# Kernel tuning notes

Measured on AMD Instinct MI355X. Metric: run time of the kernel, lower is better.

The kernel has to match this reference:

```python
import jax, jax.numpy as jnp
import numpy as np
from jax import lax

DIM, D_INNER, D_STATE, D_CONV, DT_RANK = 256, 512, 16, 4, 16
B_, H_, W_ = 4, 64, 64


def setup_inputs() -> dict:
    key = jax.random.key(0)
    ks = jax.random.split(key, 10)
    s = lambda k, shape, scale: (jax.random.normal(k, shape, dtype=jnp.float32) * scale)
    inp = {
        "x": s(ks[0], (B_, DIM, H_, W_), 1.0),
        "in_proj_w": s(ks[1], (2 * D_INNER, DIM), DIM ** -0.5),
        "conv_w": s(ks[2], (D_INNER, 1, D_CONV), D_CONV ** -0.5),
        "conv_b": s(ks[3], (D_INNER,), 0.02),
        "x_proj_w": s(ks[4], (DT_RANK + 2 * D_STATE, D_INNER), D_INNER ** -0.5),
        "dt_proj_w": s(ks[5], (D_INNER, DT_RANK), DT_RANK ** -0.5),
        "dt_proj_b": s(ks[6], (D_INNER,), 0.02),
        # A_log init: log(arange(1..d_state)) broadcast over channels (standard S4D-real init)
        "A_log": jnp.broadcast_to(jnp.log(jnp.arange(1, D_STATE + 1, dtype=jnp.float32)), (D_INNER, D_STATE)).copy(),
        "D": jnp.ones((D_INNER,), dtype=jnp.float32),
        "out_proj_w": s(ks[7], (DIM, D_INNER), D_INNER ** -0.5),
    }
    return inp


def _mamba_forward(x, in_proj_w, conv_w, conv_b, x_proj_w, dt_proj_w, dt_proj_b, A_log, D, out_proj_w):
    b, c, h, w = x.shape
    L = h * w
    xs = x.reshape(b, c, L).transpose(0, 2, 1)                      # [b, L, dim]

    xz = jnp.einsum('bld,ed->ble', xs, in_proj_w)                   # [b, L, 2*d_inner]
    u, res = jnp.split(xz, 2, axis=-1)                              # each [b, L, d_inner]

    # causal depthwise conv1d over sequence
    u_t = u.transpose(0, 2, 1)                                      # [b, d_inner, L]
    u_t = lax.conv_general_dilated(u_t, conv_w, window_strides=(1,),
                                   padding=[(D_CONV - 1, 0)],
                                   feature_group_count=D_INNER,
                                   dimension_numbers=('NCH', 'OIH', 'NCH'))
    u = jax.nn.silu(u_t.transpose(0, 2, 1) + conv_b)                # [b, L, d_inner]

    dbc = jnp.einsum('bld,ed->ble', u, x_proj_w)                    # [b, L, dt_rank+2n]
    dt, Bm, Cm = jnp.split(dbc, [DT_RANK, DT_RANK + D_STATE], axis=-1)
    delta = jax.nn.softplus(jnp.einsum('blr,dr->bld', dt, dt_proj_w) + dt_proj_b)  # [b,L,d_inner]

    A = -jnp.exp(A_log)                                             # [d_inner, n]
    deltaA = jnp.exp(jnp.einsum('bld,dn->bldn', delta, A))          # [b,L,d,n]
    deltaBu = jnp.einsum('bld,bln,bld->bldn', delta, Bm, u)         # [b,L,d,n]

    def step(state, inp):
        dA, dBu, c_t = inp                                          # [b,d,n],[b,d,n],[b,n]
        state = dA * state + dBu
        y = jnp.einsum('bdn,bn->bd', state, c_t)
        return state, y

    init = jnp.zeros((b, D_INNER, D_STATE), dtype=x.dtype)
    _, ys = lax.scan(step, init, (jnp.moveaxis(deltaA, 1, 0),
                                  jnp.moveaxis(deltaBu, 1, 0),
                                  jnp.moveaxis(Cm, 1, 0)))
    y = jnp.moveaxis(ys, 0, 1) + u * D                              # [b, L, d_inner]
    y = y * jax.nn.silu(res)
    out = jnp.einsum('ble,de->bld', y, out_proj_w)                  # [b, L, dim]
    return out.transpose(0, 2, 1).reshape(b, c, h, w)


def reference(x, in_proj_w, conv_w, conv_b, x_proj_w, dt_proj_w, dt_proj_b, A_log, D, out_proj_w):
    return _mamba_forward(x, in_proj_w, conv_w, conv_b, x_proj_w, dt_proj_w, dt_proj_b, A_log, D, out_proj_w)
```

## Files before the change

kernel.cpp:

```cpp
#include <hip/hip_runtime.h>
#include <math.h>


namespace {
constexpr int kB   = 4;
constexpr int kDim = 256;
constexpr int kL   = 4096;
constexpr int kDI  = 512;
constexpr int kN   = 16;
constexpr int kNC  = 64;
constexpr int kCS  = 64;
}

typedef __attribute__((ext_vector_type(8))) short bf16x8;
typedef __attribute__((ext_vector_type(4))) float f32x4;
typedef __attribute__((ext_vector_type(2))) float f32x2;

__device__ __forceinline__ float rcpf(float x) { return __builtin_amdgcn_rcpf(x); }
__device__ __forceinline__ float siluf(float x) { return x * rcpf(1.f + __expf(-x)); }
__device__ __forceinline__ float softplusf(float x) {
  return fmaxf(x, 0.f) + __logf(1.f + __expf(-fabsf(x)));
}

__device__ __forceinline__ unsigned short f2bf(float x) {
  union { float f; unsigned int u; } v; v.f = x;
  unsigned int u = v.u;
  u += 0x7fffu + ((u >> 16) & 1u);
  return (unsigned short)(u >> 16);
}
__device__ __forceinline__ float bf2f(unsigned short u) {
  union { unsigned int i; float f; } v; v.i = ((unsigned int)u) << 16; return v.f;
}

__device__ __forceinline__ void gload_lds16(const void* g, void* l) {
  __builtin_amdgcn_global_load_lds(
      (const __attribute__((address_space(1))) unsigned int*)g,
      (__attribute__((address_space(3))) unsigned int*)l, 16, 0, 0);
}

__global__ __launch_bounds__(256) void k_prep(const float* __restrict__ w_in,
                                              const float* __restrict__ w_out,
                                              const float* __restrict__ w_x,
                                              const float* __restrict__ w_dt,
                                              const float* __restrict__ A_log,
                                              const float* __restrict__ x,
                                              unsigned short* __restrict__ wib,
                                              unsigned short* __restrict__ wob,
                                              unsigned short* __restrict__ wxb,
                                              unsigned short* __restrict__ wdtb,
                                              float* __restrict__ Avz,
                                              unsigned int* __restrict__ flagA,
                                              unsigned short* __restrict__ xt) {
  __shared__ float Xs[64][65];
  const int blk = blockIdx.x;
  const int t = threadIdx.x;
  if (blk < 1760) {
    int idx = blk * 256 + t;
    if (idx < 262144) wib[idx] = f2bf(w_in[idx]);
    else if (idx < 393216) wob[idx - 262144] = f2bf(w_out[idx - 262144]);
    else if (idx < 417792) wxb[idx - 393216] = f2bf(w_x[idx - 393216]);
    else {
      int i = idx - 417792;
      int r = i & 31, d = i >> 5;
      wdtb[i] = (r < 16) ? f2bf(w_dt[d * 16 + r]) : (unsigned short)0;
    }
  } else if (blk < 1762) {
    int d = (blk - 1760) * 256 + t;
    float a0 = -__expf(A_log[d * kN]);
    bool ok = true;
#pragma unroll
    for (int n = 1; n < kN; ++n) {
      float av = -__expf(A_log[d * kN + n]);
      ok = ok && (fabsf(av - (n + 1) * a0) <= 1e-5f * fabsf(av));
    }
    Avz[d] = a0;
    unsigned long long bal = __ballot(ok);
    int wv = t >> 6;
    if ((t & 63) == 0) ((unsigned long long*)Xs)[wv] = bal;
    __syncthreads();
    if (t == 0) {
      unsigned long long all = ~0ull;
#pragma unroll
      for (int w = 0; w < 4; ++w) all &= ((unsigned long long*)Xs)[w];
      flagA[blk - 1760] = (all == ~0ull) ? 1u : 0u;
    }
  } else {
    int id = blk - 1762;
    int lb = id & 63, db = (id >> 6) & 3, b = id >> 8;
    const int d0 = db * 64, l0 = lb * 64;
    {
      int lq = (t & 15) * 4;
      int dr = t >> 4;
#pragma unroll
      for (int rep = 0; rep < 4; ++rep) {
        int dd = rep * 16 + dr;
        float4 v = *(const float4*)&x[((size_t)b * kDim + d0 + dd) * kL + l0 + lq];
        Xs[dd][lq] = v.x; Xs[dd][lq + 1] = v.y;
        Xs[dd][lq + 2] = v.z; Xs[dd][lq + 3] = v.w;
      }
    }
    __syncthreads();
    {
      int di = (t & 15) * 4;
      int lr = t >> 4;
#pragma unroll
      for (int rep = 0; rep < 4; ++rep) {
        int lj = rep * 16 + lr;
        ushort4 o;
        o.x = f2bf(Xs[di][lj]);     o.y = f2bf(Xs[di + 1][lj]);
        o.z = f2bf(Xs[di + 2][lj]); o.w = f2bf(Xs[di + 3][lj]);
        *(ushort4*)(xt + ((size_t)b * kL + l0 + lj) * kDim + d0 + di) = o;
      }
    }
  }
}

__global__ __launch_bounds__(256) void gemm_in_lm(const unsigned short* __restrict__ xt,
                                                  const unsigned short* __restrict__ W,
                                                  unsigned short* __restrict__ ubf,
                                                  unsigned short* __restrict__ resb) {
  __shared__ __align__(16) unsigned short As[128 * 64];
  __shared__ __align__(16) unsigned short Bs[128 * 64];
  const int e0 = blockIdx.x * 128;
  const int l0 = blockIdx.y * 128;
  const int b  = blockIdx.z;
  const int t  = threadIdx.x;
  const int wave = t >> 6, lane = t & 63;
  const int wm = wave >> 1, wn = wave & 1;
  const unsigned short* Ab = xt + (size_t)b * kL * kDim;

  f32x4 acc[4][4];
#pragma unroll
  for (int i = 0; i < 4; ++i)
#pragma unroll
    for (int j = 0; j < 4; ++j) acc[i][j] = (f32x4)0.0f;

  const int srow = t >> 3, sch = t & 7;
  for (int kt = 0; kt < 4; ++kt) {
    const int k0 = kt * 64;
#pragma unroll
    for (int c = 0; c < 4; ++c) {
      int row = c * 32 + srow;
      int gch = sch ^ (row & 7);
      gload_lds16(Ab + (size_t)(l0 + row) * kDim + k0 + gch * 8,
                  (char*)As + c * 4096 + wave * 1024);
      gload_lds16(W  + (size_t)(e0 + row) * kDim + k0 + gch * 8,
                  (char*)Bs + c * 4096 + wave * 1024);
    }
    __syncthreads();
#pragma unroll
    for (int ks = 0; ks < 2; ++ks) {
      bf16x8 af[4], bfr[4];
#pragma unroll
      for (int f = 0; f < 4; ++f) {
        int ra = wm * 64 + f * 16 + (lane & 15);
        int ca = (ks * 4 + (lane >> 4)) ^ (ra & 7);
        af[f] = *(const bf16x8*)((const char*)As + ra * 128 + ca * 16);
        int rb = wn * 64 + f * 16 + (lane & 15);
        int cb = (ks * 4 + (lane >> 4)) ^ (rb & 7);
        bfr[f] = *(const bf16x8*)((const char*)Bs + rb * 128 + cb * 16);
      }
#pragma unroll
      for (int i = 0; i < 4; ++i)
#pragma unroll
        for (int j = 0; j < 4; ++j)
          acc[i][j] = __builtin_amdgcn_mfma_f32_16x16x32_bf16(af[i], bfr[j], acc[i][j], 0, 0, 0);
    }
    __syncthreads();
  }

  const bool is_u = (e0 < kDI);
  unsigned short* dst = is_u ? ubf : resb;
  const int ebase = is_u ? e0 : (e0 - kDI);
#pragma unroll
  for (int i = 0; i < 4; ++i)
#pragma unroll
    for (int j = 0; j < 4; ++j)
#pragma unroll
      for (int r = 0; r < 4; ++r) {
        int l = l0 + wm * 64 + i * 16 + (lane >> 4) * 4 + r;
        int e = ebase + wn * 64 + j * 16 + (lane & 15);
        dst[((size_t)b * kL + l) * kDI + e] = f2bf(acc[i][j][r]);
      }
}

__global__ __launch_bounds__(256) void k_xproj_dt(const unsigned short* __restrict__ Wx,
                                                  const unsigned short* __restrict__ Wdtb,
                                                  const float* __restrict__ bdt,
                                                  const unsigned short* __restrict__ ubf,
                                                  const float* __restrict__ cw,
                                                  const float* __restrict__ cb,
                                                  float* __restrict__ dbcBC,
                                                  unsigned short* __restrict__ ucb,
                                                  unsigned short* __restrict__ delb) {
  __shared__ __align__(16) unsigned short As[64 * 64];
  __shared__ __align__(16) unsigned short Bs[64 * 64];
  __shared__ __align__(16) unsigned short dtTl[64 * 32];
  __shared__ __align__(16) unsigned short Wl[128 * 32];
  const int l0 = blockIdx.x * 64;
  const int b  = blockIdx.y;
  const int t  = threadIdx.x;
  const int wave = t >> 6, lane = t & 63;
  const unsigned short* Ub = ubf + (size_t)b * kL * kDI;

  f32x4 acc[3];
#pragma unroll
  for (int i = 0; i < 3; ++i) acc[i] = (f32x4)0.0f;

  const int srow = t >> 3, sch = t & 7;
  for (int kt = 0; kt < 8; ++kt) {
    const int k0 = kt * 64;
#pragma unroll
    for (int c = 0; c < 2; ++c) {
      int row = c * 32 + srow;
      int grow = row < 48 ? row : 47;
      int gch = sch ^ (row & 7);
      gload_lds16(Wx + (size_t)grow * kDI + k0 + gch * 8,
                  (char*)As + c * 4096 + wave * 1024);
    }
#pragma unroll
    for (int c = 0; c < 2; ++c) {
      int row = c * 32 + srow;
      int gch = sch ^ (row & 7);
      int gl = l0 + row;
      int d0 = k0 + gch * 8;
      const unsigned short* base = Ub + (size_t)gl * kDI + d0;
      uint4 zero4 = make_uint4(0, 0, 0, 0);
      uint4 c0v = *(const uint4*)base;
      uint4 c1v = (gl >= 1) ? *(const uint4*)(base - kDI)     : zero4;
      uint4 c2v = (gl >= 2) ? *(const uint4*)(base - 2 * kDI) : zero4;
      uint4 c3v = (gl >= 3) ? *(const uint4*)(base - 3 * kDI) : zero4;
      const unsigned int* p0 = (const unsigned int*)&c0v;
      const unsigned int* p1 = (const unsigned int*)&c1v;
      const unsigned int* p2 = (const unsigned int*)&c2v;
      const unsigned int* p3 = (const unsigned int*)&c3v;
      unsigned short ov[8];
#pragma unroll
      for (int cc = 0; cc < 8; ++cc) {
        int q = cc >> 1, hi = cc & 1;
        float u0 = bf2f((unsigned short)(hi ? (p0[q] >> 16) : (p0[q] & 0xffff)));
        float u1 = bf2f((unsigned short)(hi ? (p1[q] >> 16) : (p1[q] & 0xffff)));
        float u2 = bf2f((unsigned short)(hi ? (p2[q] >> 16) : (p2[q] & 0xffff)));
        float u3 = bf2f((unsigned short)(hi ? (p3[q] >> 16) : (p3[q] & 0xffff)));
        float4 w = *(const float4*)(cw + (d0 + cc) * 4);
        float a = cb[d0 + cc] + w.x * u3 + w.y * u2 + w.z * u1 + w.w * u0;
        ov[cc] = f2bf(siluf(a));
      }
      *(uint4*)((char*)Bs + c * 4096 + t * 16) = *(const uint4*)ov;
      *(uint4*)(ucb + ((size_t)b * kL + gl) * kDI + d0) = *(const uint4*)ov;
    }
    __syncthreads();
#pragma unroll
    for (int ks = 0; ks < 2; ++ks) {
      bf16x8 af[3], bfr;
#pragma unroll
      for (int f = 0; f < 3; ++f) {
        int ra = f * 16 + (lane & 15);
        int ca = (ks * 4 + (lane >> 4)) ^ (ra & 7);
        af[f] = *(const bf16x8*)((const char*)As + ra * 128 + ca * 16);
      }
      int rb = wave * 16 + (lane & 15);
      int cbk = (ks * 4 + (lane >> 4)) ^ (rb & 7);
      bfr = *(const bf16x8*)((const char*)Bs + rb * 128 + cbk * 16);
#pragma unroll
      for (int i = 0; i < 3; ++i)
        acc[i] = __builtin_amdgcn_mfma_f32_16x16x32_bf16(af[i], bfr, acc[i], 0, 0, 0);
    }
    __syncthreads();
  }

#pragma unroll
  for (int i = 1; i < 3; ++i)
#pragma unroll
    for (int r = 0; r < 4; ++r) {
      int m = i * 16 + (lane >> 4) * 4 + r;
      int l = l0 + wave * 16 + (lane & 15);
      dbcBC[((size_t)b * 32 + (m - 16)) * kL + l] = acc[i][r];
    }
  {
    int lloc = wave * 16 + (lane & 15);
    int m0 = (lane >> 4) * 4;
    ushort4 v;
    v.x = f2bf(acc[0][0]); v.y = f2bf(acc[0][1]);
    v.z = f2bf(acc[0][2]); v.w = f2bf(acc[0][3]);
    int byte = lloc * 64 + (((m0 >> 3) ^ (lloc & 3)) << 4) + ((m0 & 7) << 1);
    *(ushort4*)((char*)dtTl + byte) = v;
  }
  if (t < 128) {
    int lz = t >> 1, zc = 2 + (t & 1);
    *(uint4*)((char*)dtTl + lz * 64 + ((zc ^ (lz & 3)) << 4)) = make_uint4(0, 0, 0, 0);
  }
  __syncthreads();

  for (int dt4 = 0; dt4 < 4; ++dt4) {
#pragma unroll
    for (int c2 = 0; c2 < 2; ++c2) {
      int unit = c2 * 256 + t;
      int row = unit >> 2, sc = unit & 3;
      int gch = sc ^ (row & 3);
      gload_lds16(Wdtb + (size_t)(dt4 * 128 + row) * 32 + gch * 8,
                  (char*)Wl + c2 * 4096 + t * 16);
    }
    __syncthreads();
    f32x4 acc2[4][2];
#pragma unroll
    for (int i = 0; i < 4; ++i)
#pragma unroll
      for (int j = 0; j < 2; ++j) acc2[i][j] = (f32x4)0.0f;
    bf16x8 afr[4], bfr2[2];
#pragma unroll
    for (int f = 0; f < 4; ++f) {
      int ra = f * 16 + (lane & 15);
      afr[f] = *(const bf16x8*)((const char*)dtTl + ra * 64 + (((lane >> 4) ^ (ra & 3)) << 4));
    }
#pragma unroll
    for (int f = 0; f < 2; ++f) {
      int rb = wave * 32 + f * 16 + (lane & 15);
      bfr2[f] = *(const bf16x8*)((const char*)Wl + rb * 64 + (((lane >> 4) ^ (rb & 3)) << 4));
    }
#pragma unroll
    for (int i = 0; i < 4; ++i)
#pragma unroll
      for (int j = 0; j < 2; ++j)
        acc2[i][j] = __builtin_amdgcn_mfma_f32_16x16x32_bf16(afr[i], bfr2[j], acc2[i][j], 0, 0, 0);
#pragma unroll
    for (int j = 0; j < 2; ++j) {
      int d = dt4 * 128 + wave * 32 + j * 16 + (lane & 15);
      float bd = bdt[d];
#pragma unroll
      for (int i = 0; i < 4; ++i)
#pragma unroll
        for (int r = 0; r < 4; ++r) {
          int l = l0 + i * 16 + (lane >> 4) * 4 + r;
          float delta = softplusf(acc2[i][j][r] + bd);
          delb[((size_t)b * kL + l) * kDI + d] = f2bf(delta);
        }
    }
    __syncthreads();
  }
}

__global__ __launch_bounds__(128) void k_scanA(const unsigned short* __restrict__ delb,
                                               const unsigned short* __restrict__ ucb,
                                               const float* __restrict__ dbcBC,
                                               const float* __restrict__ A_log,
                                               const float* __restrict__ Avz,
                                               const unsigned int* __restrict__ flagA,
                                               float* __restrict__ Pprod,
                                               float* __restrict__ Pfull,
                                               float* __restrict__ S) {
  __shared__ __align__(16) float Bsh[16][kCS];
  const int b = blockIdx.z, ch = blockIdx.y;
  const int t = threadIdx.x;
  const int d = blockIdx.x * 128 + t;
  const int l0 = ch * kCS;
  {
    int row = t >> 3, li = (t & 7) * 8;
    *(float4*)&Bsh[row][li] =
        *(const float4*)&dbcBC[((size_t)b * 32 + row) * kL + l0 + li];
    *(float4*)&Bsh[row][li + 4] =
        *(const float4*)&dbcBC[((size_t)b * 32 + row) * kL + l0 + li + 4];
  }
  __syncthreads();
  const bool fast = (flagA[0] != 0u) && (flagA[1] != 0u);
  const float Av0 = Avz[d];
  const unsigned short* pDel = delb + ((size_t)b * kL + l0) * kDI + d;
  const unsigned short* pU = ucb + ((size_t)b * kL + l0) * kDI + d;
  size_t obase = (size_t)(b * kNC + ch) * (kN * kDI) + d;

  if (fast) {
    f32x2 Sv2[8];
#pragma unroll
    for (int m = 0; m < 8; ++m) Sv2[m] = (f32x2){0.f, 0.f};
    float Pp = 1.f;
    for (int i = 0; i < kCS; i += 4) {
      f32x2 a2[4], e2[4], du2[4];
#pragma unroll
      for (int jj = 0; jj < 4; ++jj) {
        float dl = bf2f(pDel[(size_t)(i + jj) * kDI]);
        float uu = bf2f(pU[(size_t)(i + jj) * kDI]);
        float E = __expf(dl * Av0);
        float duv = dl * uu;
        du2[jj] = (f32x2){duv, duv};
        float Esq = E * E;
        a2[jj] = (f32x2){E, Esq};
        e2[jj] = (f32x2){Esq, Esq};
        Pp *= E;
      }
#pragma unroll
      for (int m = 0; m < 8; ++m) {
        float4 Ba = *(const float4*)&Bsh[2 * m][i];
        float4 Bb = *(const float4*)&Bsh[2 * m + 1][i];
        Sv2[m] = Sv2[m] * a2[0] + du2[0] * (f32x2){Ba.x, Bb.x};
        Sv2[m] = Sv2[m] * a2[1] + du2[1] * (f32x2){Ba.y, Bb.y};
        Sv2[m] = Sv2[m] * a2[2] + du2[2] * (f32x2){Ba.z, Bb.z};
        Sv2[m] = Sv2[m] * a2[3] + du2[3] * (f32x2){Ba.w, Bb.w};
        if (m < 7) {
          a2[0] *= e2[0]; a2[1] *= e2[1]; a2[2] *= e2[2]; a2[3] *= e2[3];
        }
      }
    }
    Pprod[(size_t)(b * kNC + ch) * kDI + d] = Pp;
#pragma unroll
    for (int n = 0; n < kN; ++n)
      S[obase + (size_t)n * kDI] = (n & 1) ? Sv2[n >> 1].y : Sv2[n >> 1].x;
  } else {
    float Av[16];
#pragma unroll
    for (int n = 0; n < kN; ++n) Av[n] = -__expf(A_log[d * kN + n]);
    float Pv[16], Sv[16];
#pragma unroll
    for (int n = 0; n < kN; ++n) { Pv[n] = 1.f; Sv[n] = 0.f; }
    for (int i = 0; i < kCS; i += 4) {
      float del[4], du[4];
#pragma unroll
      for (int jj = 0; jj < 4; ++jj) {
        del[jj] = bf2f(pDel[(size_t)(i + jj) * kDI]);
        du[jj] = del[jj] * bf2f(pU[(size_t)(i + jj) * kDI]);
      }
#pragma unroll
      for (int n = 0; n < kN; ++n) {
        float4 B4 = *(const float4*)&Bsh[n][i];
        float a;
        a = __expf(del[0] * Av[n]); Pv[n] *= a; Sv[n] = Sv[n] * a + du[0] * B4.x;
        a = __expf(del[1] * Av[n]); Pv[n] *= a; Sv[n] = Sv[n] * a + du[1] * B4.y;
        a = __expf(del[2] * Av[n]); Pv[n] *= a; Sv[n] = Sv[n] * a + du[2] * B4.z;
        a = __expf(del[3] * Av[n]); Pv[n] *= a; Sv[n] = Sv[n] * a + du[3] * B4.w;
      }
    }
#pragma unroll
    for (int n = 0; n < kN; ++n) {
      Pfull[obase + (size_t)n * kDI] = Pv[n];
      S[obase + (size_t)n * kDI] = Sv[n];
    }
  }
}

__global__ __launch_bounds__(64) void k_scanB(const float* __restrict__ Pprod,
                                              const float* __restrict__ Pfull,
                                              const float* __restrict__ S,
                                              const unsigned int* __restrict__ flagA,
                                              float* __restrict__ init) {
  int idx = blockIdx.x * 64 + threadIdx.x;
  int b = idx >> 13, nd = idx & 8191;
  int n = nd >> 9, d = nd & 511;
  size_t base = (size_t)b * kNC * 8192 + nd;
  const bool fast = (flagA[0] != 0u) && (flagA[1] != 0u);
  float carry = 0.f;
  if (fast) {
    size_t pbase = (size_t)b * kNC * kDI + d;
    const int e = n + 1;
    for (int c0 = 0; c0 < kNC; c0 += 8) {
      float p[8], s[8];
#pragma unroll
      for (int j = 0; j < 8; ++j) {
        float pr = Pprod[pbase + (size_t)(c0 + j) * kDI];
        float p2 = pr * pr, p4 = p2 * p2, p8 = p4 * p4;
        float pw = 1.f;
        if (e & 1) pw *= pr;
        if (e & 2) pw *= p2;
        if (e & 4) pw *= p4;
        if (e & 8) pw *= p8;
        if (e & 16) pw *= p8 * p8;
        p[j] = pw;
        s[j] = S[base + (size_t)(c0 + j) * 8192];
      }
#pragma unroll
      for (int j = 0; j < 8; ++j) {
        init[base + (size_t)(c0 + j) * 8192] = carry;
        carry = p[j] * carry + s[j];
      }
    }
  } else {
    for (int c0 = 0; c0 < kNC; c0 += 8) {
      float p[8], s[8];
#pragma unroll
      for (int j = 0; j < 8; ++j) {
        size_t o = base + (size_t)(c0 + j) * 8192;
        p[j] = Pfull[o]; s[j] = S[o];
      }
#pragma unroll
      for (int j = 0; j < 8; ++j) {
        init[base + (size_t)(c0 + j) * 8192] = carry;
        carry = p[j] * carry + s[j];
      }
    }
  }
}

__global__ __launch_bounds__(128) void k_scanC(const unsigned short* __restrict__ delb,
                                               const unsigned short* __restrict__ ucb,
                                               const float* __restrict__ dbcBC,
                                               const float* __restrict__ A_log,
                                               const float* __restrict__ Avz,
                                               const unsigned int* __restrict__ flagA,
                                               const float* __restrict__ init,
                                               const unsigned short* __restrict__ resb,
                                               const float* __restrict__ Dp,
                                               unsigned short* __restrict__ yt) {
  __shared__ __align__(16) float BCsh[32][kCS];
  const int b = blockIdx.z, ch = blockIdx.y;
  const int t = threadIdx.x;
  const int d = blockIdx.x * 128 + t;
  const int l0 = ch * kCS;
  {
    int row = t >> 2, li = (t & 3) * 16;
#pragma unroll
    for (int q = 0; q < 4; ++q)
      *(float4*)&BCsh[row][li + q * 4] =
          *(const float4*)&dbcBC[((size_t)b * 32 + row) * kL + l0 + li + q * 4];
  }
  __syncthreads();
  const bool fast = (flagA[0] != 0u) && (flagA[1] != 0u);
  const float Av0 = Avz[d];
  const float Dv = Dp[d];
  const unsigned short* pDel = delb + ((size_t)b * kL + l0) * kDI + d;
  const unsigned short* pU = ucb + ((size_t)b * kL + l0) * kDI + d;
  const unsigned short* pR = resb + ((size_t)b * kL + l0) * kDI + d;
  unsigned short* pY = yt + ((size_t)b * kL + l0) * kDI + d;
  size_t ibase = (size_t)(b * kNC + ch) * (kN * kDI) + d;

  if (fast) {
    f32x2 s2[8];
#pragma unroll
    for (int m = 0; m < 8; ++m)
      s2[m] = (f32x2){init[ibase + (size_t)(2 * m) * kDI],
                      init[ibase + (size_t)(2 * m + 1) * kDI]};
    for (int i = 0; i < kCS; i += 4) {
      float uv[4];
      f32x2 a2[4], e2[4], du2[4], yacc2[4];
#pragma unroll
      for (int jj = 0; jj < 4; ++jj) {
        float dl = bf2f(pDel[(size_t)(i + jj) * kDI]);
        uv[jj] = bf2f(pU[(size_t)(i + jj) * kDI]);
        float E = __expf(dl * Av0);
        float duv = dl * uv[jj];
        du2[jj] = (f32x2){duv, duv};
        float Esq = E * E;
        a2[jj] = (f32x2){E, Esq};
        e2[jj] = (f32x2){Esq, Esq};
        yacc2[jj] = (f32x2){0.f, 0.f};
      }
#pragma unroll
      for (int m = 0; m < 8; ++m) {
        float4 Ba = *(const float4*)&BCsh[2 * m][i];
        float4 Bb = *(const float4*)&BCsh[2 * m + 1][i];
        float4 Ca = *(const float4*)&BCsh[16 + 2 * m][i];
        float4 Cb = *(const float4*)&BCsh[16 + 2 * m + 1][i];
        s2[m] = s2[m] * a2[0] + du2[0] * (f32x2){Ba.x, Bb.x};
        yacc2[0] = yacc2[0] + s2[m] * (f32x2){Ca.x, Cb.x};
        s2[m] = s2[m] * a2[1] + du2[1] * (f32x2){Ba.y, Bb.y};
        yacc2[1] = yacc2[1] + s2[m] * (f32x2){Ca.y, Cb.y};
        s2[m] = s2[m] * a2[2] + du2[2] * (f32x2){Ba.z, Bb.z};
        yacc2[2] = yacc2[2] + s2[m] * (f32x2){Ca.z, Cb.z};
        s2[m] = s2[m] * a2[3] + du2[3] * (f32x2){Ba.w, Bb.w};
        yacc2[3] = yacc2[3] + s2[m] * (f32x2){Ca.w, Cb.w};
        if (m < 7) {
          a2[0] *= e2[0]; a2[1] *= e2[1]; a2[2] *= e2[2]; a2[3] *= e2[3];
        }
      }
#pragma unroll
      for (int jj = 0; jj < 4; ++jj) {
        float yv = yacc2[jj].x + yacc2[jj].y;
        float r = bf2f(pR[(size_t)(i + jj) * kDI]);
        float gv = (yv + uv[jj] * Dv) * siluf(r);
        pY[(size_t)(i + jj) * kDI] = f2bf(gv);
      }
    }
  } else {
    float Av[16];
#pragma unroll
    for (int n = 0; n < kN; ++n) Av[n] = -__expf(A_log[d * kN + n]);
    float s[16];
#pragma unroll
    for (int n = 0; n < kN; ++n) s[n] = init[ibase + (size_t)n * kDI];
    for (int i = 0; i < kCS; i += 4) {
      float uv[4], du[4], del[4], yacc[4] = {0.f, 0.f, 0.f, 0.f};
#pragma unroll
      for (int jj = 0; jj < 4; ++jj) {
        del[jj] = bf2f(pDel[(size_t)(i + jj) * kDI]);
        uv[jj] = bf2f(pU[(size_t)(i + jj) * kDI]);
        du[jj] = del[jj] * uv[jj];
      }
#pragma unroll
      for (int n = 0; n < kN; ++n) {
        float4 B4 = *(const float4*)&BCsh[n][i];
        float4 C4 = *(const float4*)&BCsh[16 + n][i];
        float a;
        a = __expf(del[0] * Av[n]); s[n] = s[n] * a + du[0] * B4.x; yacc[0] += s[n] * C4.x;
        a = __expf(del[1] * Av[n]); s[n] = s[n] * a + du[1] * B4.y; yacc[1] += s[n] * C4.y;
        a = __expf(del[2] * Av[n]); s[n] = s[n] * a + du[2] * B4.z; yacc[2] += s[n] * C4.z;
        a = __expf(del[3] * Av[n]); s[n] = s[n] * a + du[3] * B4.w; yacc[3] += s[n] * C4.w;
      }
#pragma unroll
      for (int jj = 0; jj < 4; ++jj) {
        float r = bf2f(pR[(size_t)(i + jj) * kDI]);
        float gv = (yacc[jj] + uv[jj] * Dv) * siluf(r);
        pY[(size_t)(i + jj) * kDI] = f2bf(gv);
      }
    }
  }
}

__global__ __launch_bounds__(256) void gemm_out(const unsigned short* __restrict__ A,
                                                const unsigned short* __restrict__ Bt,
                                                float* __restrict__ C0) {
  __shared__ __align__(16) unsigned short As[128 * 64];
  __shared__ __align__(16) unsigned short Bs[128 * 64];
  const int n0 = blockIdx.x * 128;
  const int m0 = blockIdx.y * 128;
  const int b  = blockIdx.z;
  const int t  = threadIdx.x;
  const int wave = t >> 6, lane = t & 63;
  const int wm = wave >> 1, wn = wave & 1;
  const unsigned short* Bb = Bt + (size_t)b * kL * kDI;

  f32x4 acc[4][4];
#pragma unroll
  for (int i = 0; i < 4; ++i)
#pragma unroll
    for (int j = 0; j < 4; ++j) acc[i][j] = (f32x4)0.0f;

  const int srow = t >> 3, sch = t & 7;
  for (int kt = 0; kt < 8; ++kt) {
    const int k0 = kt * 64;
#pragma unroll
    for (int c = 0; c < 4; ++c) {
      int row = c * 32 + srow;
      int gch = sch ^ (row & 7);
      gload_lds16(A  + (size_t)(m0 + row) * kDI + k0 + gch * 8,
                  (char*)As + c * 4096 + wave * 1024);
      gload_lds16(Bb + (size_t)(n0 + row) * kDI + k0 + gch * 8,
                  (char*)Bs + c * 4096 + wave * 1024);
    }
    __syncthreads();
#pragma unroll
    for (int ks = 0; ks < 2; ++ks) {
      bf16x8 af[4], bfr[4];
#pragma unroll
      for (int f = 0; f < 4; ++f) {
        int ra = wm * 64 + f * 16 + (lane & 15);
        int ca = (ks * 4 + (lane >> 4)) ^ (ra & 7);
        af[f] = *(const bf16x8*)((const char*)As + ra * 128 + ca * 16);
        int rb = wn * 64 + f * 16 + (lane & 15);
        int cb = (ks * 4 + (lane >> 4)) ^ (rb & 7);
        bfr[f] = *(const bf16x8*)((const char*)Bs + rb * 128 + cb * 16);
      }
#pragma unroll
      for (int i = 0; i < 4; ++i)
#pragma unroll
        for (int j = 0; j < 4; ++j)
          acc[i][j] = __builtin_amdgcn_mfma_f32_16x16x32_bf16(af[i], bfr[j], acc[i][j], 0, 0, 0);
    }
    __syncthreads();
  }
#pragma unroll
  for (int i = 0; i < 4; ++i)
#pragma unroll
    for (int j = 0; j < 4; ++j)
#pragma unroll
      for (int r = 0; r < 4; ++r) {
        int m = m0 + wm * 64 + i * 16 + (lane >> 4) * 4 + r;
        int n = n0 + wn * 64 + j * 16 + (lane & 15);
        C0[((size_t)b * kDim + m) * kL + n] = acc[i][j][r];
      }
}

extern "C" void kernel_launch(void* const* d_in, const int* in_sizes, int n_in,
                              void* d_out, int out_size, void* d_ws, size_t ws_size,
                              hipStream_t stream) {
  const float* x       = (const float*)d_in[0];
  const float* in_w    = (const float*)d_in[1];
  const float* conv_w  = (const float*)d_in[2];
  const float* conv_b  = (const float*)d_in[3];
  const float* xproj_w = (const float*)d_in[4];
  const float* dt_w    = (const float*)d_in[5];
  const float* dt_b    = (const float*)d_in[6];
  const float* A_log   = (const float*)d_in[7];
  const float* Dp      = (const float*)d_in[8];
  const float* out_w   = (const float*)d_in[9];
  float* out = (float*)d_out;

  float* ws = (float*)d_ws;
  const size_t nBLD  = (size_t)kB * kL * kDI;
  const size_t nPS   = (size_t)kB * kNC * kN * kDI;
  float* dbcBC  = ws;
  float* Sb     = dbcBC + 524288;
  float* initb  = Sb + nPS;
  float* Pprodb = initb + nPS;
  unsigned short* ubf  = (unsigned short*)(Pprodb + 131072);
  unsigned short* ucb  = ubf + nBLD;
  unsigned short* resb = ucb + nBLD;
  unsigned short* delb = resb + nBLD;
  unsigned short* wib  = delb + nBLD;
  unsigned short* wob  = wib + 262144;
  unsigned short* wxb  = wob + 131072;
  unsigned short* wdtb = wxb + 24576;
  float* Avz           = (float*)(wdtb + 32768);
  unsigned int* flagA  = (unsigned int*)(Avz + 512);
  unsigned short* xt   = delb;
  float* Pfull         = (float*)ubf;
  unsigned short* yt   = (unsigned short*)ubf;

  k_prep<<<dim3(2786), 256, 0, stream>>>(in_w, out_w, xproj_w, dt_w, A_log, x,
                                         wib, wob, wxb, wdtb, Avz, flagA, xt);
  gemm_in_lm<<<dim3(8, kL / 128, kB), 256, 0, stream>>>(xt, wib, ubf, resb);
  k_xproj_dt<<<dim3(kL / 64, kB), 256, 0, stream>>>(wxb, wdtb, dt_b, ubf, conv_w, conv_b,
                                                    dbcBC, ucb, delb);
  k_scanA<<<dim3(4, kNC, kB), 128, 0, stream>>>(delb, ucb, dbcBC, A_log, Avz, flagA, Pprodb, Pfull, Sb);
  k_scanB<<<dim3(kB * kDI * kN / 64), 64, 0, stream>>>(Pprodb, Pfull, Sb, flagA, initb);
  k_scanC<<<dim3(4, kNC, kB), 128, 0, stream>>>(delb, ucb, dbcBC, A_log, Avz, flagA, initb, resb, Dp, yt);
  gemm_out<<<dim3(kL / 128, kDim / 128, kB), 256, 0, stream>>>(wob, yt, out);
}
```

Baseline: 131.7 us.

## Fuse all stages into one cooperative persistent kernel with grid syncs

Replaces the seven separate kernel launches with a single cooperative persistent kernel. Each stage loops over its jobs with a grid-stride loop, and stages are separated by grid.sync(). The dt projection is split into its own GEMM stage using a new dtT workspace buffer. This removes launch gaps and inter-kernel drain, but the grid is capped at 512 blocks, so stages such as the 1024-tile input GEMM and the 2786-job prep need several passes. Grid-wide barriers and the launch_bounds occupancy hint may also cost throughput.

```diff
diff --git a/kernel.cpp b/kernel.cpp
--- a/kernel.cpp
+++ b/kernel.cpp
@@ -1,6 +1,9 @@
 #include <hip/hip_runtime.h>
+#include <hip/hip_cooperative_groups.h>
 #include <math.h>
 
+
+namespace cg = cooperative_groups;
 
 namespace {
 constexpr int kB   = 4;
@@ -89,8 +92,7 @@
     int lb = id & 63, db = (id >> 6) & 3, b = id >> 8;
     const int d0 = db * 64, l0 = lb * 64;
     {
-      int lq = (t & 15) * 4;
-      int dr = t >> 4;
+      int lq = (t & 15) * 4, dr = t >> 4;
 #pragma unroll
       for (int rep = 0; rep < 4; ++rep) {
         int dd = rep * 16 + dr;
@@ -101,8 +103,7 @@
     }
     __syncthreads();
     {
-      int di = (t & 15) * 4;
-      int lr = t >> 4;
+      int di = (t & 15) * 4, lr = t >> 4;
 #pragma unroll
       for (int rep = 0; rep < 4; ++rep) {
         int lj = rep * 16 + lr;
@@ -666,6 +667,623 @@
       }
 }
 
+struct MegaArgs {
+  const float* x;
+  const float* w_in;
+  const float* cw;
+  const float* cb;
+  const float* w_x;
+  const float* w_dt;
+  const float* bdt;
+  const float* A_log;
+  const float* Dp;
+  const float* w_out;
+  float* out;
+  float* dbcBC;
+  float* Sb;
+  float* initb;
+  float* Pprodb;
+  unsigned short* ubf;
+  unsigned short* ucb;
+  unsigned short* resb;
+  unsigned short* delb;
+  unsigned short* wib;
+  unsigned short* wob;
+  unsigned short* wxb;
+  unsigned short* wdtb;
+  unsigned short* dtT;
+  float* Avz;
+  unsigned int* flagA;
+  unsigned short* xt;
+  float* Pfull;
+  unsigned short* yt;
+};
+
+union SMem {
+  struct { unsigned short As[128 * 64]; unsigned short Bs[128 * 64]; } gin;
+  struct { unsigned short As[64 * 64];  unsigned short Bs[32 * 64];  } xp;
+  struct { unsigned short As[128 * 32]; unsigned short Bs[128 * 32]; } gdt;
+  struct { float Bsh[16][kCS]; } sa;
+  struct { float BCsh[32][kCS]; } sc;
+  struct { unsigned short As[64 * 64];  unsigned short Bs[128 * 64]; } go;
+  float Xs[64][65];
+};
+
+__global__ __launch_bounds__(256, 2) void k_mega(MegaArgs a) {
+  __shared__ SMem sm;
+  cg::grid_group grid = cg::this_grid();
+  const int nblk = gridDim.x;
+  const int t = threadIdx.x;
+  const int wave = t >> 6, lane = t & 63;
+
+  for (int job = blockIdx.x; job < 2786; job += nblk) {
+    __syncthreads();
+    if (job < 1760) {
+      int idx = job * 256 + t;
+      if (idx < 262144) a.wib[idx] = f2bf(a.w_in[idx]);
+      else if (idx < 393216) a.wob[idx - 262144] = f2bf(a.w_out[idx - 262144]);
+      else if (idx < 417792) a.wxb[idx - 393216] = f2bf(a.w_x[idx - 393216]);
+      else {
+        int i = idx - 417792;
+        int r = i & 31, d = i >> 5;
+        a.wdtb[i] = (r < 16) ? f2bf(a.w_dt[d * 16 + r]) : (unsigned short)0;
+      }
+    } else if (job < 1762) {
+      int d = (job - 1760) * 256 + t;
+      float a0 = -__expf(a.A_log[d * kN]);
+      bool ok = true;
+#pragma unroll
+      for (int n = 1; n < kN; ++n) {
+        float av = -__expf(a.A_log[d * kN + n]);
+        ok = ok && (fabsf(av - (n + 1) * a0) <= 1e-5f * fabsf(av));
+      }
+      a.Avz[d] = a0;
+      unsigned long long bal = __ballot(ok);
+      if ((t & 63) == 0) ((unsigned long long*)sm.Xs)[wave] = bal;
+      __syncthreads();
+      if (t == 0) {
+        unsigned long long all = ~0ull;
+#pragma unroll
+        for (int w = 0; w < 4; ++w) all &= ((unsigned long long*)sm.Xs)[w];
+        a.flagA[job - 1760] = (all == ~0ull) ? 1u : 0u;
+      }
+    } else {
+      int id = job - 1762;
+      int lb = id & 63, db = (id >> 6) & 3, b = id >> 8;
+      const int d0 = db * 64, l0 = lb * 64;
+      {
+        int lq = (t & 15) * 4, dr = t >> 4;
+#pragma unroll
+        for (int rep = 0; rep < 4; ++rep) {
+          int dd = rep * 16 + dr;
+          float4 v = *(const float4*)&a.x[((size_t)b * kDim + d0 + dd) * kL + l0 + lq];
+          sm.Xs[dd][lq] = v.x; sm.Xs[dd][lq + 1] = v.y;
+          sm.Xs[dd][lq + 2] = v.z; sm.Xs[dd][lq + 3] = v.w;
+        }
+      }
+      __syncthreads();
+      {
+        int di = (t & 15) * 4, lr = t >> 4;
+#pragma unroll
+        for (int rep = 0; rep < 4; ++rep) {
+          int lj = rep * 16 + lr;
+          ushort4 o;
+          o.x = f2bf(sm.Xs[di][lj]);     o.y = f2bf(sm.Xs[di + 1][lj]);
+          o.z = f2bf(sm.Xs[di + 2][lj]); o.w = f2bf(sm.Xs[di + 3][lj]);
+          *(ushort4*)(a.xt + ((size_t)b * kL + l0 + lj) * kDim + d0 + di) = o;
+        }
+      }
+    }
+  }
+  grid.sync();
+
+  for (int job = blockIdx.x; job < 1024; job += nblk) {
+    const int e0 = (job & 7) * 128;
+    const int l0 = ((job >> 3) & 31) * 128;
+    const int b  = job >> 8;
+    const unsigned short* Ab = a.xt + (size_t)b * kL * kDim;
+    f32x4 acc[4][4];
+#pragma unroll
+    for (int i = 0; i < 4; ++i)
+#pragma unroll
+      for (int j = 0; j < 4; ++j) acc[i][j] = (f32x4)0.0f;
+    const int srow = t >> 3, sch = t & 7;
+    const int wm = wave >> 1, wn = wave & 1;
+    __syncthreads();
+    for (int kt = 0; kt < 4; ++kt) {
+      const int k0 = kt * 64;
+#pragma unroll
+      for (int c = 0; c < 4; ++c) {
+        int row = c * 32 + srow;
+        int gch = sch ^ (row & 7);
+        gload_lds16(Ab + (size_t)(l0 + row) * kDim + k0 + gch * 8,
+                    (char*)sm.gin.As + c * 4096 + wave * 1024);
+        gload_lds16(a.wib + (size_t)(e0 + row) * kDim + k0 + gch * 8,
+                    (char*)sm.gin.Bs + c * 4096 + wave * 1024);
+      }
+      __syncthreads();
+#pragma unroll
+      for (int ks = 0; ks < 2; ++ks) {
+        bf16x8 af[4], bfr[4];
+#pragma unroll
+        for (int f = 0; f < 4; ++f) {
+          int ra = wm * 64 + f * 16 + (lane & 15);
+          int ca = (ks * 4 + (lane >> 4)) ^ (ra & 7);
+          af[f] = *(const bf16x8*)((const char*)sm.gin.As + ra * 128 + ca * 16);
+          int rb = wn * 64 + f * 16 + (lane & 15);
+          int cb = (ks * 4 + (lane >> 4)) ^ (rb & 7);
+          bfr[f] = *(const bf16x8*)((const char*)sm.gin.Bs + rb * 128 + cb * 16);
+        }
+#pragma unroll
+        for (int i = 0; i < 4; ++i)
+#pragma unroll
+          for (int j = 0; j < 4; ++j)
+            acc[i][j] = __builtin_amdgcn_mfma_f32_16x16x32_bf16(af[i], bfr[j], acc[i][j], 0, 0, 0);
+      }
+      __syncthreads();
+    }
+    const bool is_u = (e0 < kDI);
+    unsigned short* dst = is_u ? a.ubf : a.resb;
+    const int ebase = is_u ? e0 : (e0 - kDI);
+#pragma unroll
+    for (int i = 0; i < 4; ++i)
+#pragma unroll
+      for (int j = 0; j < 4; ++j)
+#pragma unroll
+        for (int r = 0; r < 4; ++r) {
+          int l = l0 + wm * 64 + i * 16 + (lane >> 4) * 4 + r;
+          int e = ebase + wn * 64 + j * 16 + (lane & 15);
+          dst[((size_t)b * kL + l) * kDI + e] = f2bf(acc[i][j][r]);
+        }
+  }
+  grid.sync();
+
+  for (int job = blockIdx.x; job < 512; job += nblk) {
+    const int l0 = (job & 127) * 32;
+    const int b  = job >> 7;
+    const unsigned short* Ub = a.ubf + (size_t)b * kL * kDI;
+    f32x4 acc[3];
+#pragma unroll
+    for (int i = 0; i < 3; ++i) acc[i] = (f32x4)0.0f;
+    const int srow = t >> 3, sch = t & 7;
+    __syncthreads();
+    for (int kt = 0; kt < 8; ++kt) {
+      const int k0 = kt * 64;
+#pragma unroll
+      for (int c = 0; c < 2; ++c) {
+        int row = c * 32 + srow;
+        int grow = row < 48 ? row : 47;
+        int gch = sch ^ (row & 7);
+        gload_lds16(a.wxb + (size_t)grow * kDI + k0 + gch * 8,
+                    (char*)sm.xp.As + c * 4096 + wave * 1024);
+      }
+      {
+        int row = srow;
+        int gch = sch ^ (row & 7);
+        int gl = l0 + row;
+        int d0 = k0 + gch * 8;
+        const unsigned short* base = Ub + (size_t)gl * kDI + d0;
+        uint4 zero4 = make_uint4(0, 0, 0, 0);
+        uint4 c0v = *(const uint4*)base;
+        uint4 c1v = (gl >= 1) ? *(const uint4*)(base - kDI)     : zero4;
+        uint4 c2v = (gl >= 2) ? *(const uint4*)(base - 2 * kDI) : zero4;
+        uint4 c3v = (gl >= 3) ? *(const uint4*)(base - 3 * kDI) : zero4;
+        const unsigned int* p0 = (const unsigned int*)&c0v;
+        const unsigned int* p1 = (const unsigned int*)&c1v;
+        const unsigned int* p2 = (const unsigned int*)&c2v;
+        const unsigned int* p3 = (const unsigned int*)&c3v;
+        unsigned short ov[8];
+#pragma unroll
+        for (int cc = 0; cc < 8; ++cc) {
+          int q = cc >> 1, hi = cc & 1;
+          float u0 = bf2f((unsigned short)(hi ? (p0[q] >> 16) : (p0[q] & 0xffff)));
+          float u1 = bf2f((unsigned short)(hi ? (p1[q] >> 16) : (p1[q] & 0xffff)));
+          float u2 = bf2f((unsigned short)(hi ? (p2[q] >> 16) : (p2[q] & 0xffff)));
+          float u3 = bf2f((unsigned short)(hi ? (p3[q] >> 16) : (p3[q] & 0xffff)));
+          float4 w = *(const float4*)(a.cw + (d0 + cc) * 4);
+          float av = a.cb[d0 + cc] + w.x * u3 + w.y * u2 + w.z * u1 + w.w * u0;
+          ov[cc] = f2bf(siluf(av));
+        }
+        *(uint4*)((char*)sm.xp.Bs + t * 16) = *(const uint4*)ov;
+        *(uint4*)(a.ucb + ((size_t)b * kL + gl) * kDI + d0) = *(const uint4*)ov;
+      }
+      __syncthreads();
+      if (wave < 2) {
+#pragma unroll
+        for (int ks = 0; ks < 2; ++ks) {
+          bf16x8 af[3], bfr;
+#pragma unroll
+          for (int f = 0; f < 3; ++f) {
+            int ra = f * 16 + (lane & 15);
+            int ca = (ks * 4 + (lane >> 4)) ^ (ra & 7);
+            af[f] = *(const bf16x8*)((const char*)sm.xp.As + ra * 128 + ca * 16);
+          }
+          int rb = wave * 16 + (lane & 15);
+          int cbk = (ks * 4 + (lane >> 4)) ^ (rb & 7);
+          bfr = *(const bf16x8*)((const char*)sm.xp.Bs + rb * 128 + cbk * 16);
+#pragma unroll
+          for (int i = 0; i < 3; ++i)
+            acc[i] = __builtin_amdgcn_mfma_f32_16x16x32_bf16(af[i], bfr, acc[i], 0, 0, 0);
+        }
+      }
+      __syncthreads();
+    }
+    if (wave < 2) {
+      int l = l0 + wave * 16 + (lane & 15);
+#pragma unroll
+      for (int i = 1; i < 3; ++i)
+#pragma unroll
+        for (int r = 0; r < 4; ++r) {
+          int m = i * 16 + (lane >> 4) * 4 + r;
+          a.dbcBC[((size_t)b * 32 + (m - 16)) * kL + l] = acc[i][r];
+        }
+      int m0 = (lane >> 4) * 4;
+      ushort4 v;
+      v.x = f2bf(acc[0][0]); v.y = f2bf(acc[0][1]);
+      v.z = f2bf(acc[0][2]); v.w = f2bf(acc[0][3]);
+      *(ushort4*)(a.dtT + ((size_t)b * kL + l) * 32 + m0) = v;
+      *(ushort4*)(a.dtT + ((size_t)b * kL + l) * 32 + 16 + m0) = make_ushort4(0, 0, 0, 0);
+    }
+  }
+  grid.sync();
+
+  for (int job = blockIdx.x; job < 512; job += nblk) {
+    const int n0 = (job & 3) * 128;
+    const int l0 = ((job >> 2) & 31) * 128;
+    const int b  = job >> 7;
+    const unsigned short* Ab = a.dtT + (size_t)b * kL * 32;
+    __syncthreads();
+#pragma unroll
+    for (int c = 0; c < 2; ++c) {
+      int unit = c * 256 + t;
+      int row = unit >> 2, sc = unit & 3;
+      int gch = sc ^ (row & 3);
+      gload_lds16(Ab + (size_t)(l0 + row) * 32 + gch * 8,
+                  (char*)sm.gdt.As + c * 4096 + t * 16);
+      gload_lds16(a.wdtb + (size_t)(n0 + row) * 32 + gch * 8,
+                  (char*)sm.gdt.Bs + c * 4096 + t * 16);
+    }
+    __syncthreads();
+    f32x4 acc[4][4];
+#pragma unroll
+    for (int i = 0; i < 4; ++i)
+#pragma unroll
+      for (int j = 0; j < 4; ++j) acc[i][j] = (f32x4)0.0f;
+    const int wm = wave >> 1, wn = wave & 1;
+    bf16x8 af[4], bfr[4];
+#pragma unroll
+    for (int f = 0; f < 4; ++f) {
+      int ra = wm * 64 + f * 16 + (lane & 15);
+      int ca = (lane >> 4) ^ (ra & 3);
+      af[f] = *(const bf16x8*)((const char*)sm.gdt.As + ra * 64 + ca * 16);
+      int rb = wn * 64 + f * 16 + (lane & 15);
+      int cb = (lane >> 4) ^ (rb & 3);
+      bfr[f] = *(const bf16x8*)((const char*)sm.gdt.Bs + rb * 64 + cb * 16);
+    }
+#pragma unroll
+    for (int i = 0; i < 4; ++i)
+#pragma unroll
+      for (int j = 0; j < 4; ++j)
+        acc[i][j] = __builtin_amdgcn_mfma_f32_16x16x32_bf16(af[i], bfr[j], acc[i][j], 0, 0, 0);
+#pragma unroll
+    for (int j = 0; j < 4; ++j) {
+      int d = n0 + wn * 64 + j * 16 + (lane & 15);
+      float bd = a.bdt[d];
+#pragma unroll
+      for (int i = 0; i < 4; ++i)
+#pragma unroll
+        for (int r = 0; r < 4; ++r) {
+          int l = l0 + wm * 64 + i * 16 + (lane >> 4) * 4 + r;
+          float delta = softplusf(acc[i][j][r] + bd);
+          a.delb[((size_t)b * kL + l) * kDI + d] = f2bf(delta);
+        }
+    }
+  }
+  grid.sync();
+
+  for (int job = blockIdx.x; job < 512; job += nblk) {
+    const int dh = job & 1, ch = (job >> 1) & 63, b = job >> 7;
+    const int d = dh * 256 + t;
+    const int l0 = ch * kCS;
+    __syncthreads();
+    {
+      int row = t >> 4, li = (t & 15) * 4;
+      *(float4*)&sm.sa.Bsh[row][li] =
+          *(const float4*)&a.dbcBC[((size_t)b * 32 + row) * kL + l0 + li];
+    }
+    __syncthreads();
+    const bool fast = (a.flagA[0] != 0u) && (a.flagA[1] != 0u);
+    const float Av0 = a.Avz[d];
+    const unsigned short* pDel = a.delb + ((size_t)b * kL + l0) * kDI + d;
+    const unsigned short* pU = a.ucb + ((size_t)b * kL + l0) * kDI + d;
+    size_t obase = (size_t)(b * kNC + ch) * (kN * kDI) + d;
+    if (fast) {
+      f32x2 Sv2[8];
+#pragma unroll
+      for (int m = 0; m < 8; ++m) Sv2[m] = (f32x2){0.f, 0.f};
+      float Pp = 1.f;
+      for (int i = 0; i < kCS; i += 4) {
+        f32x2 a2[4], e2[4], du2[4];
+#pragma unroll
+        for (int jj = 0; jj < 4; ++jj) {
+          float dl = bf2f(pDel[(size_t)(i + jj) * kDI]);
+          float uu = bf2f(pU[(size_t)(i + jj) * kDI]);
+          float E = __expf(dl * Av0);
+          float duv = dl * uu;
+          du2[jj] = (f32x2){duv, duv};
+          float Esq = E * E;
+          a2[jj] = (f32x2){E, Esq};
+          e2[jj] = (f32x2){Esq, Esq};
+          Pp *= E;
+        }
+#pragma unroll
+        for (int m = 0; m < 8; ++m) {
+          float4 Ba = *(const float4*)&sm.sa.Bsh[2 * m][i];
+          float4 Bb = *(const float4*)&sm.sa.Bsh[2 * m + 1][i];
+          Sv2[m] = Sv2[m] * a2[0] + du2[0] * (f32x2){Ba.x, Bb.x};
+          Sv2[m] = Sv2[m] * a2[1] + du2[1] * (f32x2){Ba.y, Bb.y};
+          Sv2[m] = Sv2[m] * a2[2] + du2[2] * (f32x2){Ba.z, Bb.z};
+          Sv2[m] = Sv2[m] * a2[3] + du2[3] * (f32x2){Ba.w, Bb.w};
+          if (m < 7) {
+            a2[0] *= e2[0]; a2[1] *= e2[1]; a2[2] *= e2[2]; a2[3] *= e2[3];
+          }
+        }
+      }
+      a.Pprodb[(size_t)(b * kNC + ch) * kDI + d] = Pp;
+#pragma unroll
+      for (int n = 0; n < kN; ++n)
+        a.Sb[obase + (size_t)n * kDI] = (n & 1) ? Sv2[n >> 1].y : Sv2[n >> 1].x;
+    } else {
+      float Av[16];
+#pragma unroll
+      for (int n = 0; n < kN; ++n) Av[n] = -__expf(a.A_log[d * kN + n]);
+      float Pv[16], Sv[16];
+#pragma unroll
+      for (int n = 0; n < kN; ++n) { Pv[n] = 1.f; Sv[n] = 0.f; }
+      for (int i = 0; i < kCS; i += 4) {
+        float del[4], du[4];
+#pragma unroll
+        for (int jj = 0; jj < 4; ++jj) {
+          del[jj] = bf2f(pDel[(size_t)(i + jj) * kDI]);
+          du[jj] = del[jj] * bf2f(pU[(size_t)(i + jj) * kDI]);
+        }
+#pragma unroll
+        for (int n = 0; n < kN; ++n) {
+          float4 B4 = *(const float4*)&sm.sa.Bsh[n][i];
+          float v;
+          v = __expf(del[0] * Av[n]); Pv[n] *= v; Sv[n] = Sv[n] * v + du[0] * B4.x;
+          v = __expf(del[1] * Av[n]); Pv[n] *= v; Sv[n] = Sv[n] * v + du[1] * B4.y;
+          v = __expf(del[2] * Av[n]); Pv[n] *= v; Sv[n] = Sv[n] * v + du[2] * B4.z;
+          v = __expf(del[3] * Av[n]); Pv[n] *= v; Sv[n] = Sv[n] * v + du[3] * B4.w;
+        }
+      }
+#pragma unroll
+      for (int n = 0; n < kN; ++n) {
+        a.Pfull[obase + (size_t)n * kDI] = Pv[n];
+        a.Sb[obase + (size_t)n * kDI] = Sv[n];
+      }
+    }
+  }
+  grid.sync();
+
+  for (int idx = blockIdx.x * 256 + t; idx < 32768; idx += nblk * 256) {
+    int b = idx >> 13, nd = idx & 8191;
+    int n = nd >> 9, d = nd & 511;
+    size_t base = (size_t)b * kNC * 8192 + nd;
+    const bool fast = (a.flagA[0] != 0u) && (a.flagA[1] != 0u);
+    float carry = 0.f;
+    if (fast) {
+      size_t pbase = (size_t)b * kNC * kDI + d;
+      const int e = n + 1;
+      for (int c0 = 0; c0 < kNC; c0 += 8) {
+        float p[8], s[8];
+#pragma unroll
+        for (int j = 0; j < 8; ++j) {
+          float pr = a.Pprodb[pbase + (size_t)(c0 + j) * kDI];
+          float p2 = pr * pr, p4 = p2 * p2, p8 = p4 * p4;
+          float pw = 1.f;
+          if (e & 1) pw *= pr;
+          if (e & 2) pw *= p2;
+          if (e & 4) pw *= p4;
+          if (e & 8) pw *= p8;
+          if (e & 16) pw *= p8 * p8;
+          p[j] = pw;
+          s[j] = a.Sb[base + (size_t)(c0 + j) * 8192];
+        }
+#pragma unroll
+        for (int j = 0; j < 8; ++j) {
+          a.initb[base + (size_t)(c0 + j) * 8192] = carry;
+          carry = p[j] * carry + s[j];
+        }
+      }
+    } else {
+      for (int c0 = 0; c0 < kNC; c0 += 8) {
+        float p[8], s[8];
+#pragma unroll
+        for (int j = 0; j < 8; ++j) {
+          size_t o = base + (size_t)(c0 + j) * 8192;
+          p[j] = a.Pfull[o]; s[j] = a.Sb[o];
+        }
+#pragma unroll
+        for (int j = 0; j < 8; ++j) {
+          a.initb[base + (size_t)(c0 + j) * 8192] = carry;
+          carry = p[j] * carry + s[j];
+        }
+      }
+    }
+  }
+  grid.sync();
+
+  for (int job = blockIdx.x; job < 512; job += nblk) {
+    const int dh = job & 1, ch = (job >> 1) & 63, b = job >> 7;
+    const int d = dh * 256 + t;
+    const int l0 = ch * kCS;
+    __syncthreads();
+    {
+      int row = t >> 3, li = (t & 7) * 8;
+      *(float4*)&sm.sc.BCsh[row][li] =
+          *(const float4*)&a.dbcBC[((size_t)b * 32 + row) * kL + l0 + li];
+      *(float4*)&sm.sc.BCsh[row][li + 4] =
+          *(const float4*)&a.dbcBC[((size_t)b * 32 + row) * kL + l0 + li + 4];
+    }
+    __syncthreads();
+    const bool fast = (a.flagA[0] != 0u) && (a.flagA[1] != 0u);
+    const float Av0 = a.Avz[d];
+    const float Dv = a.Dp[d];
+    const unsigned short* pDel = a.delb + ((size_t)b * kL + l0) * kDI + d;
+    const unsigned short* pU = a.ucb + ((size_t)b * kL + l0) * kDI + d;
+    const unsigned short* pR = a.resb + ((size_t)b * kL + l0) * kDI + d;
+    unsigned short* pY = a.yt + ((size_t)b * kL + l0) * kDI + d;
+    size_t ibase = (size_t)(b * kNC + ch) * (kN * kDI) + d;
+    if (fast) {
+      f32x2 s2[8];
+#pragma unroll
+      for (int m = 0; m < 8; ++m)
+        s2[m] = (f32x2){a.initb[ibase + (size_t)(2 * m) * kDI],
+                        a.initb[ibase + (size_t)(2 * m + 1) * kDI]};
+      for (int i = 0; i < kCS; i += 4) {
+        float uv[4];
+        f32x2 a2[4], e2[4], du2[4], yacc2[4];
+#pragma unroll
+        for (int jj = 0; jj < 4; ++jj) {
+          float dl = bf2f(pDel[(size_t)(i + jj) * kDI]);
+          uv[jj] = bf2f(pU[(size_t)(i + jj) * kDI]);
+          float E = __expf(dl * Av0);
+          float duv = dl * uv[jj];
+          du2[jj] = (f32x2){duv, duv};
+          float Esq = E * E;
+          a2[jj] = (f32x2){E, Esq};
+          e2[jj] = (f32x2){Esq, Esq};
+          yacc2[jj] = (f32x2){0.f, 0.f};
+        }
+#pragma unroll
+        for (int m = 0; m < 8; ++m) {
+          float4 Ba = *(const float4*)&sm.sc.BCsh[2 * m][i];
+          float4 Bb = *(const float4*)&sm.sc.BCsh[2 * m + 1][i];
+          float4 Ca = *(const float4*)&sm.sc.BCsh[16 + 2 * m][i];
+          float4 Cb = *(const float4*)&sm.sc.BCsh[16 + 2 * m + 1][i];
+          s2[m] = s2[m] * a2[0] + du2[0] * (f32x2){Ba.x, Bb.x};
+          yacc2[0] = yacc2[0] + s2[m] * (f32x2){Ca.x, Cb.x};
+          s2[m] = s2[m] * a2[1] + du2[1] * (f32x2){Ba.y, Bb.y};
+          yacc2[1] = yacc2[1] + s2[m] * (f32x2){Ca.y, Cb.y};
+          s2[m] = s2[m] * a2[2] + du2[2] * (f32x2){Ba.z, Bb.z};
+          yacc2[2] = yacc2[2] + s2[m] * (f32x2){Ca.z, Cb.z};
+          s2[m] = s2[m] * a2[3] + du2[3] * (f32x2){Ba.w, Bb.w};
+          yacc2[3] = yacc2[3] + s2[m] * (f32x2){Ca.w, Cb.w};
+          if (m < 7) {
+            a2[0] *= e2[0]; a2[1] *= e2[1]; a2[2] *= e2[2]; a2[3] *= e2[3];
+          }
+        }
+#pragma unroll
+        for (int jj = 0; jj < 4; ++jj) {
+          float yv = yacc2[jj].x + yacc2[jj].y;
+          float r = bf2f(pR[(size_t)(i + jj) * kDI]);
+          float gv = (yv + uv[jj] * Dv) * siluf(r);
+          pY[(size_t)(i + jj) * kDI] = f2bf(gv);
+        }
+      }
+    } else {
+      float Av[16];
+#pragma unroll
+      for (int n = 0; n < kN; ++n) Av[n] = -__expf(a.A_log[d * kN + n]);
+      float s[16];
+#pragma unroll
+      for (int n = 0; n < kN; ++n) s[n] = a.initb[ibase + (size_t)n * kDI];
+      for (int i = 0; i < kCS; i += 4) {
+        float uv[4], du[4], del[4], yacc[4] = {0.f, 0.f, 0.f, 0.f};
+#pragma unroll
+        for (int jj = 0; jj < 4; ++jj) {
+          del[jj] = bf2f(pDel[(size_t)(i + jj) * kDI]);
+          uv[jj] = bf2f(pU[(size_t)(i + jj) * kDI]);
+          du[jj] = del[jj] * uv[jj];
+        }
+#pragma unroll
+        for (int n = 0; n < kN; ++n) {
+          float4 B4 = *(const float4*)&sm.sc.BCsh[n][i];
+          float4 C4 = *(const float4*)&sm.sc.BCsh[16 + n][i];
+          float v;
+          v = __expf(del[0] * Av[n]); s[n] = s[n] * v + du[0] * B4.x; yacc[0] += s[n] * C4.x;
+          v = __expf(del[1] * Av[n]); s[n] = s[n] * v + du[1] * B4.y; yacc[1] += s[n] * C4.y;
+          v = __expf(del[2] * Av[n]); s[n] = s[n] * v + du[2] * B4.z; yacc[2] += s[n] * C4.z;
+          v = __expf(del[3] * Av[n]); s[n] = s[n] * v + du[3] * B4.w; yacc[3] += s[n] * C4.w;
+        }
+#pragma unroll
+        for (int jj = 0; jj < 4; ++jj) {
+          float r = bf2f(pR[(size_t)(i + jj) * kDI]);
+          float gv = (yacc[jj] + uv[jj] * Dv) * siluf(r);
+          pY[(size_t)(i + jj) * kDI] = f2bf(gv);
+        }
+      }
+    }
+  }
+  grid.sync();
+
+  for (int job = blockIdx.x; job < 512; job += nblk) {
+    const int l0 = (job & 31) * 128;
+    const int c0 = ((job >> 5) & 3) * 64;
+    const int b  = job >> 7;
+    const unsigned short* Bb = a.yt + (size_t)b * kL * kDI;
+    f32x4 acc[2][4];
+#pragma unroll
+    for (int i = 0; i < 2; ++i)
+#pragma unroll
+      for (int j = 0; j < 4; ++j) acc[i][j] = (f32x4)0.0f;
+    const int srow = t >> 3, sch = t & 7;
+    const int wm = wave >> 1, wn = wave & 1;
+    __syncthreads();
+    for (int kt = 0; kt < 8; ++kt) {
+      const int k0 = kt * 64;
+#pragma unroll
+      for (int c = 0; c < 2; ++c) {
+        int row = c * 32 + srow;
+        int gch = sch ^ (row & 7);
+        gload_lds16(a.wob + (size_t)(c0 + row) * kDI + k0 + gch * 8,
+                    (char*)sm.go.As + c * 4096 + wave * 1024);
+      }
+#pragma unroll
+      for (int c = 0; c < 4; ++c) {
+        int row = c * 32 + srow;
+        int gch = sch ^ (row & 7);
+        gload_lds16(Bb + (size_t)(l0 + row) * kDI + k0 + gch * 8,
+                    (char*)sm.go.Bs + c * 4096 + wave * 1024);
+      }
+      __syncthreads();
+#pragma unroll
+      for (int ks = 0; ks < 2; ++ks) {
+        bf16x8 af[2], bfr[4];
+#pragma unroll
+        for (int f = 0; f < 2; ++f) {
+          int ra = wm * 32 + f * 16 + (lane & 15);
+          int ca = (ks * 4 + (lane >> 4)) ^ (ra & 7);
+          af[f] = *(const bf16x8*)((const char*)sm.go.As + ra * 128 + ca * 16);
+        }
+#pragma unroll
+        for (int f = 0; f < 4; ++f) {
+          int rb = wn * 64 + f * 16 + (lane & 15);
+          int cb = (ks * 4 + (lane >> 4)) ^ (rb & 7);
+          bfr[f] = *(const bf16x8*)((const char*)sm.go.Bs + rb * 128 + cb * 16);
+        }
+#pragma unroll
+        for (int i = 0; i < 2; ++i)
+#pragma unroll
+          for (int j = 0; j < 4; ++j)
+            acc[i][j] = __builtin_amdgcn_mfma_f32_16x16x32_bf16(af[i], bfr[j], acc[i][j], 0, 0, 0);
+      }
+      __syncthreads();
+    }
+#pragma unroll
+    for (int i = 0; i < 2; ++i)
+#pragma unroll
+      for (int j = 0; j < 4; ++j)
+#pragma unroll
+        for (int r = 0; r < 4; ++r) {
+          int m = c0 + wm * 32 + i * 16 + (lane >> 4) * 4 + r;
+          int n = l0 + wn * 64 + j * 16 + (lane & 15);
+          a.out[((size_t)b * kDim + m) * kL + n] = acc[i][j][r];
+        }
+  }
+}
+
 extern "C" void kernel_launch(void* const* d_in, const int* in_sizes, int n_in,
                               void* d_out, int out_size, void* d_ws, size_t ws_size,
                               hipStream_t stream) {
@@ -696,11 +1314,39 @@
   unsigned short* wob  = wib + 262144;
   unsigned short* wxb  = wob + 131072;
   unsigned short* wdtb = wxb + 24576;
-  float* Avz           = (float*)(wdtb + 32768);
+  unsigned short* dtT  = wdtb + 32768;
+  float* Avz           = (float*)(dtT + 524288);
   unsigned int* flagA  = (unsigned int*)(Avz + 512);
   unsigned short* xt   = delb;
   float* Pfull         = (float*)ubf;
   unsigned short* yt   = (unsigned short*)ubf;
+
+  int dev = 0;
+  hipGetDevice(&dev);
+  int coop = 0;
+  hipDeviceGetAttribute(&coop, hipDeviceAttributeCooperativeLaunch, dev);
+  int numCU = 0;
+  hipDeviceGetAttribute(&numCU, hipDeviceAttributeMultiprocessorCount, dev);
+  if (numCU <= 0) numCU = 256;
+  int maxBlk = 0;
+  hipOccupancyMaxActiveBlocksPerMultiprocessor(&maxBlk, (const void*)k_mega, 256, 0);
+  int grid = maxBlk * numCU;
+  if (grid > 512) grid = 512;
+
+  if (coop && grid >= 64) {
+    MegaArgs a;
+    a.x = x; a.w_in = in_w; a.cw = conv_w; a.cb = conv_b; a.w_x = xproj_w;
+    a.w_dt = dt_w; a.bdt = dt_b; a.A_log = A_log; a.Dp = Dp; a.w_out = out_w;
+    a.out = out;
+    a.dbcBC = dbcBC; a.Sb = Sb; a.initb = initb; a.Pprodb = Pprodb;
+    a.ubf = ubf; a.ucb = ucb; a.resb = resb; a.delb = delb;
+    a.wib = wib; a.wob = wob; a.wxb = wxb; a.wdtb = wdtb; a.dtT = dtT;
+    a.Avz = Avz; a.flagA = flagA; a.xt = xt; a.Pfull = Pfull; a.yt = yt;
+    void* kargs[] = { (void*)&a };
+    hipLaunchCooperativeKernel((const void*)k_mega, dim3(grid), dim3(256),
+                               kargs, 0, stream);
+    return;
+  }
 
   k_prep<<<dim3(2786), 256, 0, stream>>>(in_w, out_w, xproj_w, dt_w, A_log, x,
                                          wib, wob, wxb, wdtb, Avz, flagA, xt);
```

Measured after the change: 396.2 us. 201% more time.
